# Kernel optimization log

Hardware: AMD Instinct MI355X
Metric: run time of the kernel (lower is better)

The kernel has to match this reference:

```python
import jax, jax.numpy as jnp
import numpy as np

B, K, N, E, T = 4096, 64, 100000, 128, 3


def setup_inputs() -> dict:
    key = jax.random.key(0)
    ks = jax.random.split(key, 16)
    f = lambda i, shape: jax.random.normal(ks[i], shape, dtype=jnp.float32) * 0.05
    return dict(
        nodes=jax.random.randint(ks[0], (B,), 0, N),
        neigh_idx=jax.random.randint(ks[1], (T, B, K), 0, N),
        node_emb=f(2, (N, E)),
        node_prof=f(3, (N, E)),
        neigh_emb=f(4, (T, N, E)),
        neigh_prof=f(5, (T, N, E)),
        W_f=f(6, (2 * E, E)), b_f=jnp.zeros((E,), jnp.float32),
        Wa1=f(7, (2 * E, E)), ba1=jnp.zeros((E,), jnp.float32),
        Wa2=f(8, (E, E)), ba2=jnp.zeros((E,), jnp.float32),
        Wa3=f(9, (E, 1)), ba3=jnp.zeros((1,), jnp.float32),
        W1=f(10, (E, E)), b1=jnp.zeros((E,), jnp.float32),
        W2=f(11, (E, E)), b2=jnp.zeros((E,), jnp.float32),
        Wc=f(12, (2 * E, E)), bc=jnp.zeros((E,), jnp.float32),
        Wt=f(13, (T * E, T)),
    )


def reference(nodes, neigh_idx, node_emb, node_prof, neigh_emb, neigh_prof,
              W_f, b_f, Wa1, ba1, Wa2, ba2, Wa3, ba3,
              W1, b1, W2, b2, Wc, bc, Wt):
    # fusion(emb, profile) = relu(Linear(concat(emb, profile)))
    fuse = lambda e, p: jax.nn.relu(jnp.concatenate([e, p], -1) @ W_f + b_f)

    nodes_fusion = fuse(node_emb[nodes], node_prof[nodes])            # [B,E]

    per_type = []
    for t in range(T):                                                 # small fixed loop over types
        idx = neigh_idx[t]                                             # [B,K]
        nf = fuse(neigh_emb[t][idx], neigh_prof[t][idx])               # [B,K,E]
        # attention MLP over (neighbor, node) pairs -> softmax over K neighbors
        x = jnp.concatenate(
            [nf, jnp.broadcast_to(nodes_fusion[:, None, :], nf.shape)], -1)  # [B,K,2E]
        h = jax.nn.relu(x @ Wa1 + ba1)
        h = jax.nn.relu(h @ Wa2 + ba2)
        att = jax.nn.softmax((h @ Wa3 + ba3).squeeze(-1), axis=1)      # [B,K]
        agg = jnp.einsum('bke,bk->be', nf, att)                        # weighted neighbor sum
        per_type.append(jax.nn.relu(agg @ W1 + b1))                    # linear_1 + relu

    type_agg = jnp.concatenate(per_type, axis=1)                       # [B,T*E]
    att_t = jax.nn.softmax(type_agg @ Wt, axis=1)                      # [B,T]
    final = jnp.einsum('bte,bt->be', type_agg.reshape(B, T, E), att_t)
    final = jax.nn.relu(final @ W2 + b2)                               # linear_2 + relu
    out = jax.nn.relu(jnp.concatenate([nodes_fusion, final], 1) @ Wc + bc)
    return out, att_t[:, :, None]
```

## Files before the change

### kernel.cpp

```cpp
#include <hip/hip_runtime.h>
#include <hip/hip_bf16.h>

#define B_ 4096
#define K_ 64
#define N_ 100000
#define E_ 128
#define T_ 3

typedef __bf16 bf16x8 __attribute__((ext_vector_type(8)));
typedef float  f32x4  __attribute__((ext_vector_type(4)));

static __device__ __forceinline__ bf16x8 cvt8r(f32x4 u, f32x4 v) {
    bf16x8 o;
    o[0] = (__bf16)u[0]; o[1] = (__bf16)u[1]; o[2] = (__bf16)u[2]; o[3] = (__bf16)u[3];
    o[4] = (__bf16)v[0]; o[5] = (__bf16)v[1]; o[6] = (__bf16)v[2]; o[7] = (__bf16)v[3];
    return o;
}

typedef const __attribute__((address_space(1))) void GAS;
typedef __attribute__((address_space(3))) void LAS;
static __device__ __forceinline__ void gload16(const void* g, void* l) {
    __builtin_amdgcn_global_load_lds((GAS*)g, (LAS*)l, 16, 0, 0);
}

#define MFMA16(a, b, c) __builtin_amdgcn_mfma_f32_16x16x32_bf16((a), (b), (c), 0, 0, 0)

__global__ __launch_bounds__(256)
void k_prep(const float* __restrict__ W_f, const float* __restrict__ Wa1,
            const float* __restrict__ Wa2, const float* __restrict__ W1,
            __bf16* __restrict__ WtF, __bf16* __restrict__ Wa1t,
            __bf16* __restrict__ Wa2t, __bf16* __restrict__ W1t) {
    const int n = blockIdx.x;
    const int k = threadIdx.x;
    if (blockIdx.y == 0) {
        WtF[n * 256 + k] = (__bf16)W_f[k * 128 + n];
    } else if (blockIdx.y == 1) {
        if (k < 128) Wa1t[n * 128 + k] = (__bf16)Wa1[k * 128 + n];
    } else if (blockIdx.y == 2) {
        if (k < 128) Wa2t[n * 128 + k] = (__bf16)Wa2[k * 128 + n];
    } else {
        if (k < 128) W1t[n * 128 + k] = (__bf16)W1[k * 128 + n];
    }
}

__global__ __launch_bounds__(128)
void k_node_fusion(const int* __restrict__ nodes,
                   const float* __restrict__ node_emb,
                   const float* __restrict__ node_prof,
                   const float* __restrict__ W_f, const float* __restrict__ b_f,
                   __bf16* __restrict__ nodes_fusion) {
    __shared__ float x[256];
    const int b = blockIdx.x;
    const int e = threadIdx.x;
    const int nd = nodes[b];
    x[e]       = node_emb[(size_t)nd * E_ + e];
    x[128 + e] = node_prof[(size_t)nd * E_ + e];
    __syncthreads();
    float acc = b_f[e];
#pragma unroll 8
    for (int i = 0; i < 256; ++i) acc = fmaf(x[i], W_f[i * E_ + e], acc);
    nodes_fusion[(size_t)b * E_ + e] = (__bf16)fmaxf(acc, 0.f);
}

__global__ __launch_bounds__(128)
void k_node_pre(const __bf16* __restrict__ nodes_fusion,
                const float* __restrict__ Wa1, const float* __restrict__ ba1,
                __bf16* __restrict__ node_pre) {
    __shared__ float x[128];
    const int b = blockIdx.x;
    const int c = threadIdx.x;
    x[c] = (float)nodes_fusion[(size_t)b * E_ + c];
    __syncthreads();
    float acc = ba1[c];
#pragma unroll 8
    for (int i = 0; i < 128; ++i) acc = fmaf(x[i], Wa1[(128 + i) * E_ + c], acc);
    node_pre[(size_t)b * E_ + c] = (__bf16)acc;
}

#define NF_GRID 768
#define NF_TPT (N_ / 16)
#define NF_NJOB (NF_TPT * T_)

__global__ __launch_bounds__(256, 3)
void k_nf(const float* __restrict__ neigh_emb,
          const float* __restrict__ neigh_prof,
          const __bf16* __restrict__ WtF, const float* __restrict__ b_f,
          const __bf16* __restrict__ Wa1t,
          __bf16* __restrict__ NFt, __bf16* __restrict__ Gt) {
    __shared__ __align__(16) float  Xf[2][16 * 256];
    __shared__ __align__(16) __bf16 NFl[16 * 128];

    const int tid  = threadIdx.x;
    const int wid  = tid >> 6, lane = tid & 63;
    const int lr   = lane & 15, lk = lane >> 4;

    bf16x8 wf[16];
#pragma unroll
    for (int ks = 0; ks < 8; ++ks)
#pragma unroll
        for (int n = 0; n < 2; ++n)
            wf[ks * 2 + n] = *(const bf16x8*)&WtF[
                (size_t)(wid * 32 + n * 16 + lr) * 256 + ks * 32 + lk * 8];
    bf16x8 wa1r[8];
#pragma unroll
    for (int ks = 0; ks < 4; ++ks)
#pragma unroll
        for (int n = 0; n < 2; ++n)
            wa1r[ks * 2 + n] = *(const bf16x8*)&Wa1t[
                (size_t)(wid * 32 + n * 16 + lr) * 128 + ks * 32 + lk * 8];
    const float bb0 = b_f[wid * 32 + lr];
    const float bb1 = b_f[wid * 32 + 16 + lr];

    auto stage = [&](int j, int buf) {
        const int t    = j / NF_TPT;
        const int base = (j - t * NF_TPT) * 16;
        const float* embT  = neigh_emb  + (size_t)t * N_ * E_;
        const float* profT = neigh_prof + (size_t)t * N_ * E_;
#pragma unroll
        for (int i = 0; i < 4; ++i) {
            const int r  = wid * 4 + i;
            const int id = base + r;
            const int g  = lane ^ (r & 15);
            const float* src = (g < 32)
                ? embT  + (size_t)id * E_ + g * 4
                : profT + (size_t)id * E_ + (g - 32) * 4;
            gload16(src, (char*)&Xf[buf][0] + r * 1024);
        }
    };

    int job = blockIdx.x;
    stage(job, 0);
    int cur = 0;
    bool first = true;

    const int rr = tid >> 4, qq = tid & 15;
    const int pp = qq ^ rr;

    for (; job < NF_NJOB; job += NF_GRID) {
        const int tc    = job / NF_TPT;
        const int basec = (job - tc * NF_TPT) * 16;

        if (first) { asm volatile("s_waitcnt vmcnt(0)" ::: "memory"); first = false; }
        else       { asm volatile("s_waitcnt vmcnt(2)" ::: "memory"); }
        __builtin_amdgcn_s_barrier();
        __builtin_amdgcn_sched_barrier(0);

        const int nxt = job + NF_GRID;
        if (nxt < NF_NJOB) stage(nxt, cur ^ 1);

        const float* X = &Xf[cur][0];

        {
            f32x4 acc1[2] = {};
#pragma unroll
            for (int ks = 0; ks < 8; ++ks) {
                const int g0 = ks * 8 + lk * 2;
                const f32x4 u0 = *(const f32x4*)&X[lr * 256 + ((g0 ^ lr) << 2)];
                const f32x4 v0 = *(const f32x4*)&X[lr * 256 + (((g0 + 1) ^ lr) << 2)];
                const bf16x8 a0 = cvt8r(u0, v0);
                acc1[0] = MFMA16(a0, wf[ks * 2 + 0], acc1[0]);
                acc1[1] = MFMA16(a0, wf[ks * 2 + 1], acc1[1]);
            }
#pragma unroll
            for (int n = 0; n < 2; ++n) {
                const int c = wid * 32 + n * 16 + lr;
                const float bb = n ? bb1 : bb0;
                const int q = c >> 3, eo = c & 7;
#pragma unroll
                for (int j = 0; j < 4; ++j) {
                    const int rN = lk * 4 + j;
                    NFl[rN * 128 + ((q ^ rN) << 3) + eo] =
                        (__bf16)fmaxf(acc1[n][j] + bb, 0.f);
                }
            }
        }
        asm volatile("s_waitcnt lgkmcnt(0)" ::: "memory");
        __builtin_amdgcn_s_barrier();
        __builtin_amdgcn_sched_barrier(0);

        {
            __bf16* outp = NFt + ((size_t)tc * N_ + basec + rr) * E_ + qq * 8;
            *(bf16x8*)outp = *(const bf16x8*)&NFl[rr * 128 + (pp << 3)];
        }

        {
            f32x4 g[2] = {};
#pragma unroll
            for (int ks = 0; ks < 4; ++ks) {
                const int q = ks * 4 + lk;
                const bf16x8 a = *(const bf16x8*)&NFl[lr * 128 + ((q ^ lr) << 3)];
                g[0] = MFMA16(a, wa1r[ks * 2 + 0], g[0]);
                g[1] = MFMA16(a, wa1r[ks * 2 + 1], g[1]);
            }
            __bf16* Gl = (__bf16*)&Xf[cur][0];
#pragma unroll
            for (int n = 0; n < 2; ++n) {
                const int c = wid * 32 + n * 16 + lr;
                const int q = c >> 3, eo = c & 7;
#pragma unroll
                for (int j = 0; j < 4; ++j) {
                    const int rN = lk * 4 + j;
                    Gl[rN * 128 + ((q ^ rN) << 3) + eo] = (__bf16)g[n][j];
                }
            }
        }
        asm volatile("s_waitcnt lgkmcnt(0)" ::: "memory");
        __builtin_amdgcn_s_barrier();
        __builtin_amdgcn_sched_barrier(0);

        {
            const __bf16* Gl = (const __bf16*)&Xf[cur][0];
            __bf16* outp = Gt + ((size_t)tc * N_ + basec + rr) * E_ + qq * 8;
            *(bf16x8*)outp = *(const bf16x8*)&Gl[rr * 128 + (pp << 3)];
        }
        cur ^= 1;
    }
}

__global__ __launch_bounds__(256, 4)
void k_att(const int* __restrict__ neigh_idx,
           const __bf16* __restrict__ NFt,
           const __bf16* __restrict__ Gt,
           const __bf16* __restrict__ Wa2t,
           const float* __restrict__ ba2,
           const float* __restrict__ Wa3, const float* __restrict__ ba3,
           const __bf16* __restrict__ node_pre,
           __bf16* __restrict__ aggB) {
    __shared__ __align__(16) __bf16 Gb[64 * 128];
    __shared__ __align__(16) __bf16 Nb[64 * 128];
    __shared__ __bf16 npreL[128];
    __shared__ float  scp[128];

    const int b   = blockIdx.x;
    const int t   = blockIdx.y;
    const int tid = threadIdx.x;
    const int wid = tid >> 6, lane = tid & 63;
    const int lr = lane & 15, lk = lane >> 4;

    const int idv = neigh_idx[((size_t)t * B_ + b) * K_ + wid * 16 + lr];

    const __bf16* Gtab  = Gt  + (size_t)t * N_ * E_;
    const __bf16* NFtab = NFt + (size_t)t * N_ * E_;
#pragma unroll
    for (int i = 0; i < 4; ++i) {
        const int rowblock = wid * 16 + i * 4;
        const int rsub = i * 4 + (lane >> 4);
        const int q = (lane & 15) ^ rsub;
        const int id = __shfl(idv, rsub);
        gload16(Gtab  + (size_t)id * E_ + q * 8, (char*)Gb + rowblock * 256);
        gload16(NFtab + (size_t)id * E_ + q * 8, (char*)Nb + rowblock * 256);
    }
    if (tid < 128) npreL[tid] = node_pre[(size_t)b * E_ + tid];
    __syncthreads();

    const int mp = wid >> 1, h = wid & 1;
    f32x4 acc[2][4] = {};
#pragma unroll
    for (int ks = 0; ks < 4; ++ks) {
        const int q = ks * 4 + lk;
        const bf16x8 g0 = *(const bf16x8*)&Gb[(32 * mp + lr) * 128 + ((q ^ lr) << 3)];
        const bf16x8 g1 = *(const bf16x8*)&Gb[(32 * mp + 16 + lr) * 128 + ((q ^ lr) << 3)];
        const bf16x8 np = *(const bf16x8*)&npreL[q * 8];
        bf16x8 a0, a1;
#pragma unroll
        for (int j = 0; j < 8; ++j) {
            const float nv = (float)np[j];
            a0[j] = (__bf16)fmaxf((float)g0[j] + nv, 0.f);
            a1[j] = (__bf16)fmaxf((float)g1[j] + nv, 0.f);
        }
        const __bf16* wb = Wa2t + (size_t)(h * 64 + lr) * 128 + ks * 32 + lk * 8;
#pragma unroll
        for (int n = 0; n < 4; ++n) {
            const bf16x8 w = *(const bf16x8*)(wb + (size_t)n * 16 * 128);
            acc[0][n] = MFMA16(a0, w, acc[0][n]);
            acc[1][n] = MFMA16(a1, w, acc[1][n]);
        }
    }

    {
        float ba2r[4], wa3r[4];
#pragma unroll
        for (int n = 0; n < 4; ++n) {
            const int col = h * 64 + n * 16 + lr;
            ba2r[n] = ba2[col];
            wa3r[n] = Wa3[col];
        }
#pragma unroll
        for (int mi = 0; mi < 2; ++mi)
#pragma unroll
            for (int j = 0; j < 4; ++j) {
                float v = 0.f;
#pragma unroll
                for (int n = 0; n < 4; ++n)
                    v += fmaxf(acc[mi][n][j] + ba2r[n], 0.f) * wa3r[n];
                v += __shfl_xor(v, 1);
                v += __shfl_xor(v, 2);
                v += __shfl_xor(v, 4);
                v += __shfl_xor(v, 8);
                if (lr == 0)
                    scp[h * 64 + 32 * mp + mi * 16 + lk * 4 + j] = v;
            }
    }
    __syncthreads();

    float att;
    {
        const float v = scp[lane] + scp[64 + lane] + ba3[0];
        float m = v;
#pragma unroll
        for (int o = 32; o > 0; o >>= 1) m = fmaxf(m, __shfl_xor(m, o));
        const float pe = __expf(v - m);
        float s = pe;
#pragma unroll
        for (int o = 32; o > 0; o >>= 1) s += __shfl_xor(s, o);
        att = pe / s;
    }

    {
        const int e = wid * 32 + (lane & 31);
        const int half = lane >> 5;
        const int qe = e >> 3, eo = e & 7;
        float p = 0.f;
#pragma unroll
        for (int i = 0; i < 32; ++i) {
            const int row = half * 32 + i;
            const float av = __shfl(att, row);
            p = fmaf(av, (float)Nb[row * 128 + ((qe ^ (row & 15)) << 3) + eo], p);
        }
        p += __shfl_xor(p, 32);
        if (lane < 32)
            aggB[((size_t)b * T_ + t) * E_ + e] = (__bf16)p;
    }
}

__global__ __launch_bounds__(256)
void k_w1(const __bf16* __restrict__ aggB, const __bf16* __restrict__ W1t,
          const float* __restrict__ b1, __bf16* __restrict__ type_agg) {
    const int tid  = threadIdx.x;
    const int wid  = tid >> 6;
    const int lane = tid & 63;
    const int lr   = lane & 15;
    const int lk   = lane >> 4;
    const int rbase = blockIdx.x * 64 + wid * 16;

    f32x4 acc[8] = {};
#pragma unroll
    for (int ks = 0; ks < 4; ++ks) {
        const bf16x8 a = *(const bf16x8*)&aggB[(size_t)(rbase + lr) * 128 + ks * 32 + lk * 8];
        const __bf16* wb = W1t + (size_t)lr * 128 + ks * 32 + lk * 8;
#pragma unroll
        for (int n = 0; n < 8; ++n) {
            const bf16x8 w = *(const bf16x8*)(wb + (size_t)n * 16 * 128);
            acc[n] = MFMA16(a, w, acc[n]);
        }
    }
#pragma unroll
    for (int n = 0; n < 8; ++n) {
        const int col = n * 16 + lr;
        const float bb = b1[col];
#pragma unroll
        for (int j = 0; j < 4; ++j) {
            const int row = rbase + lk * 4 + j;
            type_agg[(size_t)row * 128 + col] = (__bf16)fmaxf(acc[n][j] + bb, 0.f);
        }
    }
}

__global__ __launch_bounds__(128)
void k_final(const __bf16* __restrict__ type_agg,
             const __bf16* __restrict__ nodes_fusion,
             const float* __restrict__ Wt,
             const float* __restrict__ W2, const float* __restrict__ b2,
             const float* __restrict__ Wc, const float* __restrict__ bc,
             float* __restrict__ out, float* __restrict__ att_out) {
    __shared__ float ta[384];
    __shared__ float nfu[128];
    __shared__ float fin[128];
    __shared__ float hb[128];
    __shared__ float att[3];
    __shared__ float red[3][128];

    const int b = blockIdx.x;
    const int e = threadIdx.x;

    const float v0 = (float)type_agg[(size_t)b * 384 + e];
    const float v1 = (float)type_agg[(size_t)b * 384 + 128 + e];
    const float v2 = (float)type_agg[(size_t)b * 384 + 256 + e];
    ta[e] = v0; ta[128 + e] = v1; ta[256 + e] = v2;
    nfu[e] = (float)nodes_fusion[(size_t)b * E_ + e];

    float p0, p1, p2;
    {
        const float* w0 = Wt + (size_t)e * 3;
        const float* w1 = Wt + (size_t)(128 + e) * 3;
        const float* w2 = Wt + (size_t)(256 + e) * 3;
        p0 = v0 * w0[0] + v1 * w1[0] + v2 * w2[0];
        p1 = v0 * w0[1] + v1 * w1[1] + v2 * w2[1];
        p2 = v0 * w0[2] + v1 * w1[2] + v2 * w2[2];
    }
    red[0][e] = p0; red[1][e] = p1; red[2][e] = p2;
    __syncthreads();

    if (e < 3) {
        float s = 0.f;
        for (int i = 0; i < 128; ++i) s += red[e][i];
        red[e][0] = s;
    }
    __syncthreads();
    if (e == 0) {
        const float s0 = red[0][0], s1 = red[1][0], s2 = red[2][0];
        const float m  = fmaxf(s0, fmaxf(s1, s2));
        const float e0 = __expf(s0 - m), e1 = __expf(s1 - m), e2 = __expf(s2 - m);
        const float inv = 1.f / (e0 + e1 + e2);
        att[0] = e0 * inv; att[1] = e1 * inv; att[2] = e2 * inv;
    }
    __syncthreads();

    fin[e] = att[0] * ta[e] + att[1] * ta[128 + e] + att[2] * ta[256 + e];
    __syncthreads();

    float acc = b2[e];
#pragma unroll 8
    for (int i = 0; i < 128; ++i) acc = fmaf(fin[i], W2[i * E_ + e], acc);
    hb[e] = fmaxf(acc, 0.f);
    __syncthreads();

    float acc2 = bc[e];
#pragma unroll 8
    for (int i = 0; i < 128; ++i) acc2 = fmaf(nfu[i], Wc[i * E_ + e], acc2);
#pragma unroll 8
    for (int i = 0; i < 128; ++i) acc2 = fmaf(hb[i], Wc[(128 + i) * E_ + e], acc2);
    out[(size_t)b * E_ + e] = fmaxf(acc2, 0.f);

    if (e < 3) att_out[(size_t)b * 3 + e] = att[e];
}

extern "C" void kernel_launch(void* const* d_in, const int* in_sizes, int n_in,
                              void* d_out, int out_size, void* d_ws, size_t ws_size,
                              hipStream_t stream) {
    const int*   nodes      = (const int*)d_in[0];
    const int*   neigh_idx  = (const int*)d_in[1];
    const float* node_emb   = (const float*)d_in[2];
    const float* node_prof  = (const float*)d_in[3];
    const float* neigh_emb  = (const float*)d_in[4];
    const float* neigh_prof = (const float*)d_in[5];
    const float* W_f = (const float*)d_in[6];  const float* b_f = (const float*)d_in[7];
    const float* Wa1 = (const float*)d_in[8];  const float* ba1 = (const float*)d_in[9];
    const float* Wa2 = (const float*)d_in[10]; const float* ba2 = (const float*)d_in[11];
    const float* Wa3 = (const float*)d_in[12]; const float* ba3 = (const float*)d_in[13];
    const float* W1  = (const float*)d_in[14]; const float* b1  = (const float*)d_in[15];
    const float* W2  = (const float*)d_in[16]; const float* b2  = (const float*)d_in[17];
    const float* Wc  = (const float*)d_in[18]; const float* bc  = (const float*)d_in[19];
    const float* Wt  = (const float*)d_in[20];

    float* out     = (float*)d_out;
    float* att_out = out + (size_t)B_ * E_;

    char* ws = (char*)d_ws;
    __bf16* nodes_fusion = (__bf16*)(ws);
    __bf16* node_pre     = (__bf16*)(ws + (1u << 20));
    __bf16* type_agg     = (__bf16*)(ws + (2u << 20));
    __bf16* aggB         = (__bf16*)(ws + (5u << 20));
    __bf16* WtF          = (__bf16*)(ws + (8u << 20));
    __bf16* Wa1t         = (__bf16*)(ws + (8u << 20) + 65536);
    __bf16* Wa2t         = (__bf16*)(ws + (8u << 20) + 98304);
    __bf16* W1t          = (__bf16*)(ws + (8u << 20) + 131072);
    __bf16* NFt          = (__bf16*)(ws + (9u << 20));
    __bf16* Gt           = (__bf16*)(ws + (83u << 20));

    k_prep<<<dim3(128, 4), 256, 0, stream>>>(W_f, Wa1, Wa2, W1, WtF, Wa1t, Wa2t, W1t);
    k_node_fusion<<<B_, 128, 0, stream>>>(nodes, node_emb, node_prof, W_f, b_f,
                                          nodes_fusion);
    k_node_pre<<<B_, 128, 0, stream>>>(nodes_fusion, Wa1, ba1, node_pre);
    k_nf<<<NF_GRID, 256, 0, stream>>>(neigh_emb, neigh_prof, WtF, b_f, Wa1t,
                                      NFt, Gt);
    k_att<<<dim3(B_, T_), 256, 0, stream>>>(neigh_idx, NFt, Gt, Wa2t, ba2,
                                            Wa3, ba3, node_pre, aggB);
    k_w1<<<(B_ * T_) / 64, 256, 0, stream>>>(aggB, W1t, b1, type_agg);
    k_final<<<B_, 128, 0, stream>>>(type_agg, nodes_fusion, Wt, W2, b2, Wc, bc,
                                    out, att_out);
}
```

Measured before the change: 302.8 us.

## Replace persistent double-buffered k_nf with one-tile-per-block grid launch

The persistent k_nf kernel, which kept weights in registers and double-buffered input tiles across a 768-block grid, becomes a non-persistent kernel that launches one block per 16-row tile per type (6250x3 blocks). Each block loads its tile once, uses plain __syncthreads, and reads the weight fragments from global memory (L2-cached) inside the MFMA loops. Shared memory per block is halved and launch bounds rise to 6 blocks per CU, so the hardware scheduler overlaps memory across blocks instead of relying on in-kernel prefetch. The cost is repeated weight loads per tile and per-block launch and prologue overhead.

```diff
diff --git a/kernel.cpp b/kernel.cpp
--- a/kernel.cpp
+++ b/kernel.cpp
@@ -77,43 +77,22 @@
     node_pre[(size_t)b * E_ + c] = (__bf16)acc;
 }
 
-#define NF_GRID 768
-#define NF_TPT (N_ / 16)
-#define NF_NJOB (NF_TPT * T_)
-
-__global__ __launch_bounds__(256, 3)
+__global__ __launch_bounds__(256, 6)
 void k_nf(const float* __restrict__ neigh_emb,
           const float* __restrict__ neigh_prof,
           const __bf16* __restrict__ WtF, const float* __restrict__ b_f,
           const __bf16* __restrict__ Wa1t,
           __bf16* __restrict__ NFt, __bf16* __restrict__ Gt) {
-    __shared__ __align__(16) float  Xf[2][16 * 256];
+    __shared__ __align__(16) float  Xf[16 * 256];
     __shared__ __align__(16) __bf16 NFl[16 * 128];
 
+    const int t    = blockIdx.y;
+    const int base = blockIdx.x * 16;
     const int tid  = threadIdx.x;
     const int wid  = tid >> 6, lane = tid & 63;
     const int lr   = lane & 15, lk = lane >> 4;
 
-    bf16x8 wf[16];
-#pragma unroll
-    for (int ks = 0; ks < 8; ++ks)
-#pragma unroll
-        for (int n = 0; n < 2; ++n)
-            wf[ks * 2 + n] = *(const bf16x8*)&WtF[
-                (size_t)(wid * 32 + n * 16 + lr) * 256 + ks * 32 + lk * 8];
-    bf16x8 wa1r[8];
-#pragma unroll
-    for (int ks = 0; ks < 4; ++ks)
-#pragma unroll
-        for (int n = 0; n < 2; ++n)
-            wa1r[ks * 2 + n] = *(const bf16x8*)&Wa1t[
-                (size_t)(wid * 32 + n * 16 + lr) * 128 + ks * 32 + lk * 8];
-    const float bb0 = b_f[wid * 32 + lr];
-    const float bb1 = b_f[wid * 32 + 16 + lr];
-
-    auto stage = [&](int j, int buf) {
-        const int t    = j / NF_TPT;
-        const int base = (j - t * NF_TPT) * 16;
+    {
         const float* embT  = neigh_emb  + (size_t)t * N_ * E_;
         const float* profT = neigh_prof + (size_t)t * N_ * E_;
 #pragma unroll
@@ -124,96 +103,80 @@
             const float* src = (g < 32)
                 ? embT  + (size_t)id * E_ + g * 4
                 : profT + (size_t)id * E_ + (g - 32) * 4;
-            gload16(src, (char*)&Xf[buf][0] + r * 1024);
-        }
-    };
-
-    int job = blockIdx.x;
-    stage(job, 0);
-    int cur = 0;
-    bool first = true;
+            gload16(src, (char*)Xf + r * 1024);
+        }
+    }
+    __syncthreads();
+
+    {
+        f32x4 acc1[2] = {};
+#pragma unroll
+        for (int ks = 0; ks < 8; ++ks) {
+            const int g0 = ks * 8 + lk * 2;
+            const f32x4 u0 = *(const f32x4*)&Xf[lr * 256 + ((g0 ^ lr) << 2)];
+            const f32x4 v0 = *(const f32x4*)&Xf[lr * 256 + (((g0 + 1) ^ lr) << 2)];
+            const bf16x8 a0 = cvt8r(u0, v0);
+#pragma unroll
+            for (int n = 0; n < 2; ++n) {
+                const bf16x8 w = *(const bf16x8*)&WtF[
+                    (size_t)(wid * 32 + n * 16 + lr) * 256 + ks * 32 + lk * 8];
+                acc1[n] = MFMA16(a0, w, acc1[n]);
+            }
+        }
+#pragma unroll
+        for (int n = 0; n < 2; ++n) {
+            const int c = wid * 32 + n * 16 + lr;
+            const float bb = b_f[c];
+            const int q = c >> 3, eo = c & 7;
+#pragma unroll
+            for (int j = 0; j < 4; ++j) {
+                const int rN = lk * 4 + j;
+                NFl[rN * 128 + ((q ^ rN) << 3) + eo] =
+                    (__bf16)fmaxf(acc1[n][j] + bb, 0.f);
+            }
+        }
+    }
+    __syncthreads();
 
     const int rr = tid >> 4, qq = tid & 15;
     const int pp = qq ^ rr;
 
-    for (; job < NF_NJOB; job += NF_GRID) {
-        const int tc    = job / NF_TPT;
-        const int basec = (job - tc * NF_TPT) * 16;
-
-        if (first) { asm volatile("s_waitcnt vmcnt(0)" ::: "memory"); first = false; }
-        else       { asm volatile("s_waitcnt vmcnt(2)" ::: "memory"); }
-        __builtin_amdgcn_s_barrier();
-        __builtin_amdgcn_sched_barrier(0);
-
-        const int nxt = job + NF_GRID;
-        if (nxt < NF_NJOB) stage(nxt, cur ^ 1);
-
-        const float* X = &Xf[cur][0];
-
-        {
-            f32x4 acc1[2] = {};
-#pragma unroll
-            for (int ks = 0; ks < 8; ++ks) {
-                const int g0 = ks * 8 + lk * 2;
-                const f32x4 u0 = *(const f32x4*)&X[lr * 256 + ((g0 ^ lr) << 2)];
-                const f32x4 v0 = *(const f32x4*)&X[lr * 256 + (((g0 + 1) ^ lr) << 2)];
-                const bf16x8 a0 = cvt8r(u0, v0);
-                acc1[0] = MFMA16(a0, wf[ks * 2 + 0], acc1[0]);
-                acc1[1] = MFMA16(a0, wf[ks * 2 + 1], acc1[1]);
+    {
+        __bf16* outp = NFt + ((size_t)t * N_ + base + rr) * E_ + qq * 8;
+        *(bf16x8*)outp = *(const bf16x8*)&NFl[rr * 128 + (pp << 3)];
+    }
+
+    {
+        f32x4 g[2] = {};
+#pragma unroll
+        for (int ks = 0; ks < 4; ++ks) {
+            const int q = ks * 4 + lk;
+            const bf16x8 a = *(const bf16x8*)&NFl[lr * 128 + ((q ^ lr) << 3)];
+#pragma unroll
+            for (int n = 0; n < 2; ++n) {
+                const bf16x8 w = *(const bf16x8*)&Wa1t[
+                    (size_t)(wid * 32 + n * 16 + lr) * 128 + ks * 32 + lk * 8];
+                g[n] = MFMA16(a, w, g[n]);
             }
-#pragma unroll
-            for (int n = 0; n < 2; ++n) {
-                const int c = wid * 32 + n * 16 + lr;
-                const float bb = n ? bb1 : bb0;
-                const int q = c >> 3, eo = c & 7;
-#pragma unroll
-                for (int j = 0; j < 4; ++j) {
-                    const int rN = lk * 4 + j;
-                    NFl[rN * 128 + ((q ^ rN) << 3) + eo] =
-                        (__bf16)fmaxf(acc1[n][j] + bb, 0.f);
-                }
+        }
+        __bf16* Gl = (__bf16*)Xf;
+#pragma unroll
+        for (int n = 0; n < 2; ++n) {
+            const int c = wid * 32 + n * 16 + lr;
+            const int q = c >> 3, eo = c & 7;
+#pragma unroll
+            for (int j = 0; j < 4; ++j) {
+                const int rN = lk * 4 + j;
+                Gl[rN * 128 + ((q ^ rN) << 3) + eo] = (__bf16)g[n][j];
             }
         }
-        asm volatile("s_waitcnt lgkmcnt(0)" ::: "memory");
-        __builtin_amdgcn_s_barrier();
-        __builtin_amdgcn_sched_barrier(0);
-
-        {
-            __bf16* outp = NFt + ((size_t)tc * N_ + basec + rr) * E_ + qq * 8;
-            *(bf16x8*)outp = *(const bf16x8*)&NFl[rr * 128 + (pp << 3)];
-        }
-
-        {
-            f32x4 g[2] = {};
-#pragma unroll
-            for (int ks = 0; ks < 4; ++ks) {
-                const int q = ks * 4 + lk;
-                const bf16x8 a = *(const bf16x8*)&NFl[lr * 128 + ((q ^ lr) << 3)];
-                g[0] = MFMA16(a, wa1r[ks * 2 + 0], g[0]);
-                g[1] = MFMA16(a, wa1r[ks * 2 + 1], g[1]);
-            }
-            __bf16* Gl = (__bf16*)&Xf[cur][0];
-#pragma unroll
-            for (int n = 0; n < 2; ++n) {
-                const int c = wid * 32 + n * 16 + lr;
-                const int q = c >> 3, eo = c & 7;
-#pragma unroll
-                for (int j = 0; j < 4; ++j) {
-                    const int rN = lk * 4 + j;
-                    Gl[rN * 128 + ((q ^ rN) << 3) + eo] = (__bf16)g[n][j];
-                }
-            }
-        }
-        asm volatile("s_waitcnt lgkmcnt(0)" ::: "memory");
-        __builtin_amdgcn_s_barrier();
-        __builtin_amdgcn_sched_barrier(0);
-
-        {
-            const __bf16* Gl = (const __bf16*)&Xf[cur][0];
-            __bf16* outp = Gt + ((size_t)tc * N_ + basec + rr) * E_ + qq * 8;
-            *(bf16x8*)outp = *(const bf16x8*)&Gl[rr * 128 + (pp << 3)];
-        }
-        cur ^= 1;
+    }
+    __syncthreads();
+
+    {
+        const __bf16* Gl = (const __bf16*)Xf;
+        __bf16* outp = Gt + ((size_t)t * N_ + base + rr) * E_ + qq * 8;
+        *(bf16x8*)outp = *(const bf16x8*)&Gl[rr * 128 + (pp << 3)];
     }
 }
 
@@ -472,8 +435,8 @@
     k_node_fusion<<<B_, 128, 0, stream>>>(nodes, node_emb, node_prof, W_f, b_f,
                                           nodes_fusion);
     k_node_pre<<<B_, 128, 0, stream>>>(nodes_fusion, Wa1, ba1, node_pre);
-    k_nf<<<NF_GRID, 256, 0, stream>>>(neigh_emb, neigh_prof, WtF, b_f, Wa1t,
-                                      NFt, Gt);
+    k_nf<<<dim3(N_ / 16, T_), 256, 0, stream>>>(neigh_emb, neigh_prof, WtF, b_f,
+                                                Wa1t, NFt, Gt);
     k_att<<<dim3(B_, T_), 256, 0, stream>>>(neigh_idx, NFt, Gt, Wa2t, ba2,
                                             Wa3, ba3, node_pre, aggB);
     k_w1<<<(B_ * T_) / 64, 256, 0, stream>>>(aggB, W1t, b1, type_agg);
```

New measurement: 427.1 us. 1.41x slower.
